# Kernel tuning notes

Hardware: AMD Instinct MI355X
Metric: run time of the kernel (lower is better)

## Reference

```python
import jax, jax.numpy as jnp
import numpy as np

HIDDEN = 128
HEADS = 8
HEAD_DIM = HIDDEN // HEADS
N_NODES = 100000
N_EDGES = 1600000


def setup_inputs() -> dict:
    key = jax.random.key(0)
    ks = jax.random.split(key, 12)
    s = 1.0 / np.sqrt(HIDDEN)
    inp = {
        "x": jax.random.normal(ks[0], (N_NODES, HIDDEN), dtype=jnp.float32),
        "edge_index": jax.random.randint(ks[1], (2, N_EDGES), 0, N_NODES, dtype=jnp.int32),
        "edge_emb": jax.random.normal(ks[2], (N_EDGES, HIDDEN), dtype=jnp.float32),
        "q_w": jax.random.uniform(ks[3], (HIDDEN, HIDDEN), jnp.float32, -s, s),
        "q_b": jax.random.uniform(ks[4], (HIDDEN,), jnp.float32, -s, s),
        "k_w": jax.random.uniform(ks[5], (HIDDEN, HIDDEN), jnp.float32, -s, s),
        "k_b": jax.random.uniform(ks[6], (HIDDEN,), jnp.float32, -s, s),
        "v_w": jax.random.uniform(ks[7], (HIDDEN, HIDDEN), jnp.float32, -s, s),
        "v_b": jax.random.uniform(ks[8], (HIDDEN,), jnp.float32, -s, s),
        "out_w": jax.random.uniform(ks[9], (HIDDEN, HIDDEN), jnp.float32, -s, s),
        "out_b": jax.random.uniform(ks[10], (HIDDEN,), jnp.float32, -s, s),
        "eb_w": jax.random.uniform(ks[11], (HEADS, HIDDEN), jnp.float32, -s, s),
        "eb_b": jnp.zeros((HEADS,), dtype=jnp.float32),
    }
    return inp


def reference(x, edge_index, edge_emb, q_w, q_b, k_w, k_b, v_w, v_b, out_w, out_b, eb_w, eb_b):
    n = x.shape[0]
    # node projections -> [N, H, D]
    q = (x @ q_w.T + q_b).reshape(n, HEADS, HEAD_DIM)
    k = (x @ k_w.T + k_b).reshape(n, HEADS, HEAD_DIM)
    v = (x @ v_w.T + v_b).reshape(n, HEADS, HEAD_DIM)

    row, col = edge_index[0], edge_index[1]
    # per-edge scores: [E, H]
    scores = jnp.einsum('ehd,ehd->eh', q[row], k[col]) / jnp.sqrt(jnp.float32(HEAD_DIM))
    scores = scores + edge_emb @ eb_w.T + eb_b

    # segmented softmax over incoming edges of each destination node `row`
    seg_max = jax.ops.segment_max(scores, row, num_segments=n)  # [N, H]
    exp_scores = jnp.exp(scores - seg_max[row])
    seg_sum = jax.ops.segment_sum(exp_scores, row, num_segments=n)  # [N, H]
    attn = exp_scores / (seg_sum[row] + 1e-10)  # [E, H]

    # weighted scatter-aggregation of values
    weighted_v = attn[..., None] * v[col]  # [E, H, D]
    out = jax.ops.segment_sum(weighted_v, row, num_segments=n)  # [N, H, D]
    out = out.reshape(n, HIDDEN)
    return out @ out_w.T + out_b
```

## Files before the change

### kernel.cpp

```cpp
#include <hip/hip_runtime.h>

#define HID 128
#define NH 8

typedef __attribute__((ext_vector_type(8))) short short8;
typedef __attribute__((ext_vector_type(4))) float f32x4;

__device__ __forceinline__ unsigned short f2bf(float f) {
    unsigned int u = __float_as_uint(f);
    u = (u + 0x7FFF + ((u >> 16) & 1)) >> 16;
    return (unsigned short)u;
}
__device__ __forceinline__ float bf2f(unsigned short s) {
    return __uint_as_float((unsigned int)s << 16);
}

__global__ void k_hist(const int* __restrict__ row, int E, int* __restrict__ count) {
    int i = blockIdx.x * blockDim.x + threadIdx.x;
    int stride = gridDim.x * blockDim.x;
    for (; i < E; i += stride) atomicAdd(&count[row[i]], 1);
}

__global__ void k_scan1(const int* __restrict__ in, int total,
                        int* __restrict__ out, int* __restrict__ bsums) {
    __shared__ int sd[256];
    int t = threadIdx.x;
    int base = blockIdx.x * 1024 + t * 4;
    int v0 = (base + 0 < total) ? in[base + 0] : 0;
    int v1 = (base + 1 < total) ? in[base + 1] : 0;
    int v2 = (base + 2 < total) ? in[base + 2] : 0;
    int v3 = (base + 3 < total) ? in[base + 3] : 0;
    int s = v0 + v1 + v2 + v3;
    sd[t] = s; __syncthreads();
    for (int off = 1; off < 256; off <<= 1) {
        int xx = (t >= off) ? sd[t - off] : 0;
        __syncthreads();
        sd[t] += xx;
        __syncthreads();
    }
    int excl = sd[t] - s;
    if (t == 255) bsums[blockIdx.x] = sd[255];
    int run = excl;
    if (base + 0 < total) out[base + 0] = run; run += v0;
    if (base + 1 < total) out[base + 1] = run; run += v1;
    if (base + 2 < total) out[base + 2] = run; run += v2;
    if (base + 3 < total) out[base + 3] = run;
}

__global__ void k_scan2(int* __restrict__ bs, int nb) {
    __shared__ int sd[128];
    int t = threadIdx.x;
    int vv = (t < nb) ? bs[t] : 0;
    sd[t] = vv; __syncthreads();
    for (int off = 1; off < 128; off <<= 1) {
        int xx = (t >= off) ? sd[t - off] : 0;
        __syncthreads();
        sd[t] += xx;
        __syncthreads();
    }
    if (t < nb) bs[t] = sd[t] - vv;
}

__global__ void k_scan3(int* __restrict__ out, int total, const int* __restrict__ bs) {
    int add = bs[blockIdx.x];
    int base = blockIdx.x * 1024 + threadIdx.x * 4;
    #pragma unroll
    for (int i = 0; i < 4; ++i)
        if (base + i < total) out[base + i] += add;
}

__global__ __launch_bounds__(256) void k_edge_fused(
    const int* __restrict__ row, const int* __restrict__ col,
    const float* __restrict__ emb, const float* __restrict__ ebw,
    const float* __restrict__ ebb, const int* __restrict__ start,
    int* __restrict__ cursor, int* __restrict__ col_sorted,
    float* __restrict__ ebias_s, int E)
{
    __shared__ float Wx[8][4][8][4];
    __shared__ float bb[8];
    int t = threadIdx.x;
    for (int i = t; i < 1024; i += 256) {
        int j = i & 3, g = (i >> 2) & 7, c = (i >> 5) & 3, h = i >> 7;
        Wx[h][c][g][j] = ebw[h * 128 + g * 16 + c * 4 + j];
    }
    if (t < 8) bb[t] = ebb[t];
    __syncthreads();

    int l = t & 63;
    int g = l & 7;
    int sub = l >> 3;
    int wid = blockIdx.x * 4 + (t >> 6);
    int nwaves = gridDim.x * 4;

    for (int base = wid * 8; base < E; base += nwaves * 8) {
        int e = base + sub;
        bool act = e < E;
        float p[8] = {0.f,0.f,0.f,0.f,0.f,0.f,0.f,0.f};
        if (act) {
            const float4* pe = (const float4*)(emb + (size_t)e * HID + g * 16);
            #pragma unroll
            for (int c = 0; c < 4; ++c) {
                float4 ev = pe[c];
                #pragma unroll
                for (int h = 0; h < 8; ++h) {
                    float4 wv = *(const float4*)&Wx[h][c][g][0];
                    p[h] += ev.x*wv.x + ev.y*wv.y + ev.z*wv.z + ev.w*wv.w;
                }
            }
        }
        #pragma unroll
        for (int off = 1; off < 8; off <<= 1) {
            #pragma unroll
            for (int h = 0; h < 8; ++h) p[h] += __shfl_xor(p[h], off);
        }
        int pslot = 0;
        if (act && g == 0) {
            int r = row[e];
            pslot = start[r] + atomicAdd(&cursor[r], 1);
            col_sorted[pslot] = col[e];
        }
        pslot = __shfl(pslot, l & 56);
        if (act) ebias_s[(size_t)pslot * NH + g] = p[g] + bb[g];
    }
}

__global__ void k_cvtw(const float* __restrict__ qw, const float* __restrict__ kw,
                       const float* __restrict__ vw, const float* __restrict__ ow,
                       unsigned short* __restrict__ wbf) {
    int i = blockIdx.x * 256 + threadIdx.x;
    int idx = i * 4;
    int m = idx >> 14;
    int off = idx & 16383;
    const float* src = (m == 0) ? qw : (m == 1) ? kw : (m == 2) ? vw : ow;
    float4 v = *(const float4*)(src + off);
    ushort4 o;
    o.x = f2bf(v.x); o.y = f2bf(v.y); o.z = f2bf(v.z); o.w = f2bf(v.w);
    *(ushort4*)(wbf + idx) = o;
}

__global__ __launch_bounds__(256) void k_qkv_mfma(
    const float* __restrict__ x, const unsigned short* __restrict__ wbf,
    const float* __restrict__ qb, const float* __restrict__ kb, const float* __restrict__ vb,
    unsigned short* __restrict__ qkvbf, int n)
{
    __shared__ unsigned short xs[64][136];
    int t = threadIdx.x;
    int m0 = blockIdx.x * 64;
    #pragma unroll
    for (int p = 0; p < 2; ++p) {
        int f = p * 256 + t;
        int r = f >> 3;
        int c16 = (f & 7) * 16;
        int node = m0 + r;
        float4 u0 = {0,0,0,0}, u1 = {0,0,0,0}, u2 = {0,0,0,0}, u3 = {0,0,0,0};
        if (node < n) {
            const float4* px = (const float4*)(x + (size_t)node * HID + c16);
            u0 = px[0]; u1 = px[1]; u2 = px[2]; u3 = px[3];
        }
        union { unsigned short u[8]; short8 v; } a, b;
        a.u[0]=f2bf(u0.x); a.u[1]=f2bf(u0.y); a.u[2]=f2bf(u0.z); a.u[3]=f2bf(u0.w);
        a.u[4]=f2bf(u1.x); a.u[5]=f2bf(u1.y); a.u[6]=f2bf(u1.z); a.u[7]=f2bf(u1.w);
        b.u[0]=f2bf(u2.x); b.u[1]=f2bf(u2.y); b.u[2]=f2bf(u2.z); b.u[3]=f2bf(u2.w);
        b.u[4]=f2bf(u3.x); b.u[5]=f2bf(u3.y); b.u[6]=f2bf(u3.z); b.u[7]=f2bf(u3.w);
        *(short8*)&xs[r][c16]     = a.v;
        *(short8*)&xs[r][c16 + 8] = b.v;
    }
    __syncthreads();

    int w = t >> 6, l = t & 63;
    int lr = l & 15, lc = l >> 4;
    short8 afr[4];
    #pragma unroll
    for (int c = 0; c < 4; ++c)
        afr[c] = *(const short8*)&xs[w * 16 + lr][c * 32 + lc * 8];

    #pragma unroll
    for (int m = 0; m < 3; ++m) {
        const float* bias = (m == 0) ? qb : (m == 1) ? kb : vb;
        #pragma unroll
        for (int ct = 0; ct < 8; ++ct) {
            int colg = ct * 16 + lr;
            f32x4 acc = {0.f, 0.f, 0.f, 0.f};
            const unsigned short* wrow = wbf + (size_t)m * 16384 + (size_t)colg * 128 + lc * 8;
            #pragma unroll
            for (int c = 0; c < 4; ++c) {
                short8 bfr = *(const short8*)(wrow + c * 32);
                acc = __builtin_amdgcn_mfma_f32_16x16x32_bf16(afr[c], bfr, acc, 0, 0, 0);
            }
            float bv = bias[colg];
            #pragma unroll
            for (int r = 0; r < 4; ++r) {
                int node = m0 + w * 16 + lc * 4 + r;
                if (node < n)
                    qkvbf[(size_t)node * 384 + m * 128 + colg] = f2bf(acc[r] + bv);
            }
        }
    }
}

__global__ __launch_bounds__(256) void k_attn(
    const unsigned short* __restrict__ qkvbf, const float* __restrict__ ebs,
    const int* __restrict__ cols, const int* __restrict__ start,
    float* __restrict__ out, int n)
{
    int node = blockIdx.x * 4 + (threadIdx.x >> 6);
    if (node >= n) return;
    int l = threadIdx.x & 63;
    int slot = l >> 3;
    int h = l & 7;
    int s0 = start[node];
    int deg = start[node + 1] - s0;

    float qf[16];
    {
        const unsigned short* qp = qkvbf + (size_t)node * 384 + h * 16;
        short8 q0 = *(const short8*)qp;
        short8 q1 = *(const short8*)(qp + 8);
        #pragma unroll
        for (int i = 0; i < 8; ++i) {
            qf[i] = bf2f((unsigned short)q0[i]);
            qf[8 + i] = bf2f((unsigned short)q1[i]);
        }
    }

    float acc[16];
    #pragma unroll
    for (int i = 0; i < 16; ++i) acc[i] = 0.f;
    float denom = 0.f;

    for (int base = 0; base < deg; base += 8) {
        int idx = base + slot;
        bool act = idx < deg;
        int c = act ? cols[s0 + idx] : 0;
        const unsigned short* kv = qkvbf + (size_t)c * 384 + 128 + h * 16;
        short8 ka  = *(const short8*)kv;
        short8 kbv = *(const short8*)(kv + 8);
        short8 va  = *(const short8*)(kv + 128);
        short8 vb  = *(const short8*)(kv + 136);
        float eb = act ? ebs[(size_t)(s0 + idx) * NH + h] : 0.f;
        float part = 0.f;
        #pragma unroll
        for (int i = 0; i < 8; ++i) part += qf[i] * bf2f((unsigned short)ka[i]);
        #pragma unroll
        for (int i = 0; i < 8; ++i) part += qf[8 + i] * bf2f((unsigned short)kbv[i]);
        float es = act ? __expf(part * 0.25f + eb) : 0.f;
        denom += es;
        #pragma unroll
        for (int i = 0; i < 8; ++i) acc[i]     += es * bf2f((unsigned short)va[i]);
        #pragma unroll
        for (int i = 0; i < 8; ++i) acc[8 + i] += es * bf2f((unsigned short)vb[i]);
    }

    #pragma unroll
    for (int off = 8; off < 64; off <<= 1) {
        denom += __shfl_xor(denom, off);
        #pragma unroll
        for (int i = 0; i < 16; ++i) acc[i] += __shfl_xor(acc[i], off);
    }
    if (slot == 0) {
        float inv = 1.f / (denom + 1e-10f);
        float* op = out + (size_t)node * HID + h * 16;
        #pragma unroll
        for (int c = 0; c < 4; ++c) {
            float4 o = make_float4(acc[c*4]*inv, acc[c*4+1]*inv, acc[c*4+2]*inv, acc[c*4+3]*inv);
            *(float4*)(op + c * 4) = o;
        }
    }
}

__global__ __launch_bounds__(256) void k_outproj_mfma(
    float* __restrict__ io, const unsigned short* __restrict__ wbf,
    const float* __restrict__ ob, int n)
{
    __shared__ unsigned short hs[64][136];
    int t = threadIdx.x;
    int m0 = blockIdx.x * 64;
    #pragma unroll
    for (int p = 0; p < 2; ++p) {
        int f = p * 256 + t;
        int r = f >> 3;
        int c16 = (f & 7) * 16;
        int node = m0 + r;
        float4 u0 = {0,0,0,0}, u1 = {0,0,0,0}, u2 = {0,0,0,0}, u3 = {0,0,0,0};
        if (node < n) {
            const float4* px = (const float4*)(io + (size_t)node * HID + c16);
            u0 = px[0]; u1 = px[1]; u2 = px[2]; u3 = px[3];
        }
        union { unsigned short u[8]; short8 v; } a, b;
        a.u[0]=f2bf(u0.x); a.u[1]=f2bf(u0.y); a.u[2]=f2bf(u0.z); a.u[3]=f2bf(u0.w);
        a.u[4]=f2bf(u1.x); a.u[5]=f2bf(u1.y); a.u[6]=f2bf(u1.z); a.u[7]=f2bf(u1.w);
        b.u[0]=f2bf(u2.x); b.u[1]=f2bf(u2.y); b.u[2]=f2bf(u2.z); b.u[3]=f2bf(u2.w);
        b.u[4]=f2bf(u3.x); b.u[5]=f2bf(u3.y); b.u[6]=f2bf(u3.z); b.u[7]=f2bf(u3.w);
        *(short8*)&hs[r][c16]     = a.v;
        *(short8*)&hs[r][c16 + 8] = b.v;
    }
    __syncthreads();

    int w = t >> 6, l = t & 63;
    int lr = l & 15, lc = l >> 4;
    short8 afr[4];
    #pragma unroll
    for (int c = 0; c < 4; ++c)
        afr[c] = *(const short8*)&hs[w * 16 + lr][c * 32 + lc * 8];

    #pragma unroll
    for (int ct = 0; ct < 8; ++ct) {
        int colg = ct * 16 + lr;
        f32x4 acc = {0.f, 0.f, 0.f, 0.f};
        const unsigned short* wrow = wbf + (size_t)3 * 16384 + (size_t)colg * 128 + lc * 8;
        #pragma unroll
        for (int c = 0; c < 4; ++c) {
            short8 bfr = *(const short8*)(wrow + c * 32);
            acc = __builtin_amdgcn_mfma_f32_16x16x32_bf16(afr[c], bfr, acc, 0, 0, 0);
        }
        float bv = ob[colg];
        #pragma unroll
        for (int r = 0; r < 4; ++r) {
            int node = m0 + w * 16 + lc * 4 + r;
            if (node < n)
                io[(size_t)node * HID + colg] = acc[r] + bv;
        }
    }
}

extern "C" void kernel_launch(void* const* d_in, const int* in_sizes, int n_in,
                              void* d_out, int out_size, void* d_ws, size_t ws_size,
                              hipStream_t stream) {
    const float* x   = (const float*)d_in[0];
    const int*   eix = (const int*)  d_in[1];
    const float* emb = (const float*)d_in[2];
    const float* qw  = (const float*)d_in[3];
    const float* qb  = (const float*)d_in[4];
    const float* kw  = (const float*)d_in[5];
    const float* kb  = (const float*)d_in[6];
    const float* vw  = (const float*)d_in[7];
    const float* vb  = (const float*)d_in[8];
    const float* ow  = (const float*)d_in[9];
    const float* ob  = (const float*)d_in[10];
    const float* ebw = (const float*)d_in[11];
    const float* ebb = (const float*)d_in[12];

    int n = in_sizes[0] / HID;
    int E = in_sizes[2] / HID;
    const int* row = eix;
    const int* col = eix + E;

    char* wsp = (char*)d_ws;
    auto alloc = [&](size_t bytes) -> void* {
        void* p = (void*)wsp;
        wsp += (bytes + 255) & ~(size_t)255;
        return p;
    };
    unsigned short* qkvbf = (unsigned short*)alloc((size_t)n * 384 * 2);
    unsigned short* wbf   = (unsigned short*)alloc((size_t)4 * 16384 * 2);
    float* ebias_s        = (float*)alloc((size_t)E * NH * 4);
    int* count            = (int*)alloc((size_t)(n + 2) * 4);
    int* startp           = (int*)alloc((size_t)(n + 2) * 4);
    int* bsums            = (int*)alloc(256 * 4);
    int* cursor           = (int*)alloc((size_t)n * 4);
    int* col_sorted       = (int*)alloc((size_t)E * 4);

    hipMemsetAsync(count, 0, (size_t)(n + 1) * sizeof(int), stream);
    hipMemsetAsync(cursor, 0, (size_t)n * sizeof(int), stream);

    k_cvtw<<<64, 256, 0, stream>>>(qw, kw, vw, ow, wbf);
    k_hist<<<2048, 256, 0, stream>>>(row, E, count);

    int total = n + 1;
    int nb = (total + 1023) / 1024;
    k_scan1<<<nb, 256, 0, stream>>>(count, total, startp, bsums);
    k_scan2<<<1, 128, 0, stream>>>(bsums, nb);
    k_scan3<<<nb, 256, 0, stream>>>(startp, total, bsums);

    k_edge_fused<<<2048, 256, 0, stream>>>(row, col, emb, ebw, ebb, startp,
                                           cursor, col_sorted, ebias_s, E);

    k_qkv_mfma<<<(n + 63) / 64, 256, 0, stream>>>(x, wbf, qb, kb, vb, qkvbf, n);
    k_attn<<<(n + 3) / 4, 256, 0, stream>>>(qkvbf, ebias_s, col_sorted, startp,
                                            (float*)d_out, n);
    k_outproj_mfma<<<(n + 63) / 64, 256, 0, stream>>>((float*)d_out, wbf, ob, n);
}
```

Baseline: 570.4 us.

## Fuse QKV projection and edge-bias pass; pack edge records, bf16 attention output

Merges the QKV projection and the edge-bias/scatter kernel into one launch with block-range dispatch, so the two independent stages run concurrently. The edge scatter now writes a 32-byte record per edge holding the column index and the eight biases as bf16, replacing the separate col_sorted and fp32 ebias arrays, so attention reads one record instead of two scattered values. Attention writes its output as bf16 into a scratch buffer that the output projection reads directly, removing an fp32 round trip and a conversion. Storing the edge bias and aggregated output in bf16 costs some precision, and the edge pass now uses one 32-edge block per launch slot instead of a grid-stride loop.

```diff
diff --git a/kernel.cpp b/kernel.cpp
--- a/kernel.cpp
+++ b/kernel.cpp
@@ -13,6 +13,9 @@
 }
 __device__ __forceinline__ float bf2f(unsigned short s) {
     return __uint_as_float((unsigned int)s << 16);
+}
+__device__ __forceinline__ unsigned int pack2bf(float lo, float hi) {
+    return (unsigned int)f2bf(lo) | ((unsigned int)f2bf(hi) << 16);
 }
 
 __global__ void k_hist(const int* __restrict__ row, int E, int* __restrict__ count) {
@@ -69,32 +72,103 @@
         if (base + i < total) out[base + i] += add;
 }
 
-__global__ __launch_bounds__(256) void k_edge_fused(
+__global__ void k_cvtw(const float* __restrict__ qw, const float* __restrict__ kw,
+                       const float* __restrict__ vw, const float* __restrict__ ow,
+                       unsigned short* __restrict__ wbf) {
+    int i = blockIdx.x * 256 + threadIdx.x;
+    int idx = i * 4;
+    int m = idx >> 14;
+    int off = idx & 16383;
+    const float* src = (m == 0) ? qw : (m == 1) ? kw : (m == 2) ? vw : ow;
+    float4 v = *(const float4*)(src + off);
+    ushort4 o;
+    o.x = f2bf(v.x); o.y = f2bf(v.y); o.z = f2bf(v.z); o.w = f2bf(v.w);
+    *(ushort4*)(wbf + idx) = o;
+}
+
+__global__ __launch_bounds__(256) void k_fat(
+    const float* __restrict__ x, const unsigned short* __restrict__ wbf,
+    const float* __restrict__ qb_, const float* __restrict__ kb_, const float* __restrict__ vb_,
+    unsigned short* __restrict__ qkvbf, int n, int qblocks,
     const int* __restrict__ row, const int* __restrict__ col,
     const float* __restrict__ emb, const float* __restrict__ ebw,
     const float* __restrict__ ebb, const int* __restrict__ start,
-    int* __restrict__ cursor, int* __restrict__ col_sorted,
-    float* __restrict__ ebias_s, int E)
+    int* __restrict__ cursor, char* __restrict__ recs, int E)
 {
-    __shared__ float Wx[8][4][8][4];
-    __shared__ float bb[8];
+    __shared__ __align__(16) char sm[17408];
+    int bid = blockIdx.x;
     int t = threadIdx.x;
-    for (int i = t; i < 1024; i += 256) {
-        int j = i & 3, g = (i >> 2) & 7, c = (i >> 5) & 3, h = i >> 7;
-        Wx[h][c][g][j] = ebw[h * 128 + g * 16 + c * 4 + j];
-    }
-    if (t < 8) bb[t] = ebb[t];
-    __syncthreads();
-
-    int l = t & 63;
-    int g = l & 7;
-    int sub = l >> 3;
-    int wid = blockIdx.x * 4 + (t >> 6);
-    int nwaves = gridDim.x * 4;
-
-    for (int base = wid * 8; base < E; base += nwaves * 8) {
-        int e = base + sub;
+
+    if (bid < qblocks) {
+        unsigned short (*xs)[136] = (unsigned short (*)[136])sm;
+        int m0 = bid * 64;
+        #pragma unroll
+        for (int p = 0; p < 2; ++p) {
+            int f = p * 256 + t;
+            int r = f >> 3;
+            int c16 = (f & 7) * 16;
+            int node = m0 + r;
+            float4 u0 = {0,0,0,0}, u1 = {0,0,0,0}, u2 = {0,0,0,0}, u3 = {0,0,0,0};
+            if (node < n) {
+                const float4* px = (const float4*)(x + (size_t)node * HID + c16);
+                u0 = px[0]; u1 = px[1]; u2 = px[2]; u3 = px[3];
+            }
+            union { unsigned short u[8]; short8 v; } a, b;
+            a.u[0]=f2bf(u0.x); a.u[1]=f2bf(u0.y); a.u[2]=f2bf(u0.z); a.u[3]=f2bf(u0.w);
+            a.u[4]=f2bf(u1.x); a.u[5]=f2bf(u1.y); a.u[6]=f2bf(u1.z); a.u[7]=f2bf(u1.w);
+            b.u[0]=f2bf(u2.x); b.u[1]=f2bf(u2.y); b.u[2]=f2bf(u2.z); b.u[3]=f2bf(u2.w);
+            b.u[4]=f2bf(u3.x); b.u[5]=f2bf(u3.y); b.u[6]=f2bf(u3.z); b.u[7]=f2bf(u3.w);
+            *(short8*)&xs[r][c16]     = a.v;
+            *(short8*)&xs[r][c16 + 8] = b.v;
+        }
+        __syncthreads();
+
+        int w = t >> 6, l = t & 63;
+        int lr = l & 15, lc = l >> 4;
+        short8 afr[4];
+        #pragma unroll
+        for (int c = 0; c < 4; ++c)
+            afr[c] = *(const short8*)&xs[w * 16 + lr][c * 32 + lc * 8];
+
+        #pragma unroll
+        for (int m = 0; m < 3; ++m) {
+            const float* bias = (m == 0) ? qb_ : (m == 1) ? kb_ : vb_;
+            #pragma unroll
+            for (int ct = 0; ct < 8; ++ct) {
+                int colg = ct * 16 + lr;
+                f32x4 acc = {0.f, 0.f, 0.f, 0.f};
+                const unsigned short* wrow = wbf + (size_t)m * 16384 + (size_t)colg * 128 + lc * 8;
+                #pragma unroll
+                for (int c = 0; c < 4; ++c) {
+                    short8 bfr = *(const short8*)(wrow + c * 32);
+                    acc = __builtin_amdgcn_mfma_f32_16x16x32_bf16(afr[c], bfr, acc, 0, 0, 0);
+                }
+                float bv = bias[colg];
+                #pragma unroll
+                for (int r = 0; r < 4; ++r) {
+                    int node = m0 + w * 16 + lc * 4 + r;
+                    if (node < n)
+                        qkvbf[(size_t)node * 384 + m * 128 + colg] = f2bf(acc[r] + bv);
+                }
+            }
+        }
+    } else {
+        float (*Wx)[4][8][4] = (float (*)[4][8][4])sm;
+        for (int i = t; i < 1024; i += 256) {
+            int j = i & 3, g = (i >> 2) & 7, c = (i >> 5) & 3, h = i >> 7;
+            Wx[h][c][g][j] = ebw[h * 128 + g * 16 + c * 4 + j];
+        }
+        float bbr[8];
+        #pragma unroll
+        for (int i = 0; i < 8; ++i) bbr[i] = ebb[i];
+        __syncthreads();
+
+        int l = t & 63;
+        int g = l & 7;
+        int sub = l >> 3;
+        int e = (bid - qblocks) * 32 + (t >> 6) * 8 + sub;
         bool act = e < E;
+
         float p[8] = {0.f,0.f,0.f,0.f,0.f,0.f,0.f,0.f};
         if (act) {
             const float4* pe = (const float4*)(emb + (size_t)e * HID + g * 16);
@@ -113,95 +187,27 @@
             #pragma unroll
             for (int h = 0; h < 8; ++h) p[h] += __shfl_xor(p[h], off);
         }
-        int pslot = 0;
         if (act && g == 0) {
             int r = row[e];
-            pslot = start[r] + atomicAdd(&cursor[r], 1);
-            col_sorted[pslot] = col[e];
-        }
-        pslot = __shfl(pslot, l & 56);
-        if (act) ebias_s[(size_t)pslot * NH + g] = p[g] + bb[g];
-    }
-}
-
-__global__ void k_cvtw(const float* __restrict__ qw, const float* __restrict__ kw,
-                       const float* __restrict__ vw, const float* __restrict__ ow,
-                       unsigned short* __restrict__ wbf) {
-    int i = blockIdx.x * 256 + threadIdx.x;
-    int idx = i * 4;
-    int m = idx >> 14;
-    int off = idx & 16383;
-    const float* src = (m == 0) ? qw : (m == 1) ? kw : (m == 2) ? vw : ow;
-    float4 v = *(const float4*)(src + off);
-    ushort4 o;
-    o.x = f2bf(v.x); o.y = f2bf(v.y); o.z = f2bf(v.z); o.w = f2bf(v.w);
-    *(ushort4*)(wbf + idx) = o;
-}
-
-__global__ __launch_bounds__(256) void k_qkv_mfma(
-    const float* __restrict__ x, const unsigned short* __restrict__ wbf,
-    const float* __restrict__ qb, const float* __restrict__ kb, const float* __restrict__ vb,
-    unsigned short* __restrict__ qkvbf, int n)
-{
-    __shared__ unsigned short xs[64][136];
-    int t = threadIdx.x;
-    int m0 = blockIdx.x * 64;
-    #pragma unroll
-    for (int p = 0; p < 2; ++p) {
-        int f = p * 256 + t;
-        int r = f >> 3;
-        int c16 = (f & 7) * 16;
-        int node = m0 + r;
-        float4 u0 = {0,0,0,0}, u1 = {0,0,0,0}, u2 = {0,0,0,0}, u3 = {0,0,0,0};
-        if (node < n) {
-            const float4* px = (const float4*)(x + (size_t)node * HID + c16);
-            u0 = px[0]; u1 = px[1]; u2 = px[2]; u3 = px[3];
-        }
-        union { unsigned short u[8]; short8 v; } a, b;
-        a.u[0]=f2bf(u0.x); a.u[1]=f2bf(u0.y); a.u[2]=f2bf(u0.z); a.u[3]=f2bf(u0.w);
-        a.u[4]=f2bf(u1.x); a.u[5]=f2bf(u1.y); a.u[6]=f2bf(u1.z); a.u[7]=f2bf(u1.w);
-        b.u[0]=f2bf(u2.x); b.u[1]=f2bf(u2.y); b.u[2]=f2bf(u2.z); b.u[3]=f2bf(u2.w);
-        b.u[4]=f2bf(u3.x); b.u[5]=f2bf(u3.y); b.u[6]=f2bf(u3.z); b.u[7]=f2bf(u3.w);
-        *(short8*)&xs[r][c16]     = a.v;
-        *(short8*)&xs[r][c16 + 8] = b.v;
-    }
-    __syncthreads();
-
-    int w = t >> 6, l = t & 63;
-    int lr = l & 15, lc = l >> 4;
-    short8 afr[4];
-    #pragma unroll
-    for (int c = 0; c < 4; ++c)
-        afr[c] = *(const short8*)&xs[w * 16 + lr][c * 32 + lc * 8];
-
-    #pragma unroll
-    for (int m = 0; m < 3; ++m) {
-        const float* bias = (m == 0) ? qb : (m == 1) ? kb : vb;
-        #pragma unroll
-        for (int ct = 0; ct < 8; ++ct) {
-            int colg = ct * 16 + lr;
-            f32x4 acc = {0.f, 0.f, 0.f, 0.f};
-            const unsigned short* wrow = wbf + (size_t)m * 16384 + (size_t)colg * 128 + lc * 8;
-            #pragma unroll
-            for (int c = 0; c < 4; ++c) {
-                short8 bfr = *(const short8*)(wrow + c * 32);
-                acc = __builtin_amdgcn_mfma_f32_16x16x32_bf16(afr[c], bfr, acc, 0, 0, 0);
-            }
-            float bv = bias[colg];
-            #pragma unroll
-            for (int r = 0; r < 4; ++r) {
-                int node = m0 + w * 16 + lc * 4 + r;
-                if (node < n)
-                    qkvbf[(size_t)node * 384 + m * 128 + colg] = f2bf(acc[r] + bv);
-            }
+            int ps = start[r] + atomicAdd(&cursor[r], 1);
+            char* rp = recs + (size_t)ps * 32;
+            uint4 r0;
+            r0.x = (unsigned int)col[e];
+            r0.y = pack2bf(p[0] + bbr[0], p[1] + bbr[1]);
+            r0.z = pack2bf(p[2] + bbr[2], p[3] + bbr[3]);
+            r0.w = pack2bf(p[4] + bbr[4], p[5] + bbr[5]);
+            uint2 r1;
+            r1.x = pack2bf(p[6] + bbr[6], p[7] + bbr[7]);
+            r1.y = 0;
+            *(uint4*)rp = r0;
+            *(uint2*)(rp + 16) = r1;
         }
     }
 }
 
 __global__ __launch_bounds__(256) void k_attn(
-    const unsigned short* __restrict__ qkvbf, const float* __restrict__ ebs,
-    const int* __restrict__ cols, const int* __restrict__ start,
-    float* __restrict__ out, int n)
+    const unsigned short* __restrict__ qkvbf, const char* __restrict__ recs,
+    const int* __restrict__ start, unsigned short* __restrict__ aout, int n)
 {
     int node = blockIdx.x * 4 + (threadIdx.x >> 6);
     if (node >= n) return;
@@ -231,13 +237,14 @@
     for (int base = 0; base < deg; base += 8) {
         int idx = base + slot;
         bool act = idx < deg;
-        int c = act ? cols[s0 + idx] : 0;
+        const char* rp = recs + (size_t)(s0 + (act ? idx : 0)) * 32;
+        int c = act ? *(const int*)rp : 0;
+        float eb = act ? bf2f(*(const unsigned short*)(rp + 4 + 2 * h)) : 0.f;
         const unsigned short* kv = qkvbf + (size_t)c * 384 + 128 + h * 16;
         short8 ka  = *(const short8*)kv;
         short8 kbv = *(const short8*)(kv + 8);
         short8 va  = *(const short8*)(kv + 128);
         short8 vb  = *(const short8*)(kv + 136);
-        float eb = act ? ebs[(size_t)(s0 + idx) * NH + h] : 0.f;
         float part = 0.f;
         #pragma unroll
         for (int i = 0; i < 8; ++i) part += qf[i] * bf2f((unsigned short)ka[i]);
@@ -259,40 +266,37 @@
     }
     if (slot == 0) {
         float inv = 1.f / (denom + 1e-10f);
-        float* op = out + (size_t)node * HID + h * 16;
-        #pragma unroll
-        for (int c = 0; c < 4; ++c) {
-            float4 o = make_float4(acc[c*4]*inv, acc[c*4+1]*inv, acc[c*4+2]*inv, acc[c*4+3]*inv);
-            *(float4*)(op + c * 4) = o;
-        }
+        uint4 o0, o1;
+        o0.x = pack2bf(acc[0]*inv,  acc[1]*inv);
+        o0.y = pack2bf(acc[2]*inv,  acc[3]*inv);
+        o0.z = pack2bf(acc[4]*inv,  acc[5]*inv);
+        o0.w = pack2bf(acc[6]*inv,  acc[7]*inv);
+        o1.x = pack2bf(acc[8]*inv,  acc[9]*inv);
+        o1.y = pack2bf(acc[10]*inv, acc[11]*inv);
+        o1.z = pack2bf(acc[12]*inv, acc[13]*inv);
+        o1.w = pack2bf(acc[14]*inv, acc[15]*inv);
+        unsigned short* op = aout + (size_t)node * HID + h * 16;
+        *(uint4*)op       = o0;
+        *(uint4*)(op + 8) = o1;
     }
 }
 
 __global__ __launch_bounds__(256) void k_outproj_mfma(
-    float* __restrict__ io, const unsigned short* __restrict__ wbf,
-    const float* __restrict__ ob, int n)
+    const unsigned short* __restrict__ aout, const unsigned short* __restrict__ wbf,
+    const float* __restrict__ ob, float* __restrict__ out, int n)
 {
     __shared__ unsigned short hs[64][136];
     int t = threadIdx.x;
     int m0 = blockIdx.x * 64;
     #pragma unroll
-    for (int p = 0; p < 2; ++p) {
+    for (int p = 0; p < 4; ++p) {
         int f = p * 256 + t;
-        int r = f >> 3;
-        int c16 = (f & 7) * 16;
+        int r = f >> 4;
+        int c8 = (f & 15) * 8;
         int node = m0 + r;
-        float4 u0 = {0,0,0,0}, u1 = {0,0,0,0}, u2 = {0,0,0,0}, u3 = {0,0,0,0};
-        if (node < n) {
-            const float4* px = (const float4*)(io + (size_t)node * HID + c16);
-            u0 = px[0]; u1 = px[1]; u2 = px[2]; u3 = px[3];
-        }
-        union { unsigned short u[8]; short8 v; } a, b;
-        a.u[0]=f2bf(u0.x); a.u[1]=f2bf(u0.y); a.u[2]=f2bf(u0.z); a.u[3]=f2bf(u0.w);
-        a.u[4]=f2bf(u1.x); a.u[5]=f2bf(u1.y); a.u[6]=f2bf(u1.z); a.u[7]=f2bf(u1.w);
-        b.u[0]=f2bf(u2.x); b.u[1]=f2bf(u2.y); b.u[2]=f2bf(u2.z); b.u[3]=f2bf(u2.w);
-        b.u[4]=f2bf(u3.x); b.u[5]=f2bf(u3.y); b.u[6]=f2bf(u3.z); b.u[7]=f2bf(u3.w);
-        *(short8*)&hs[r][c16]     = a.v;
-        *(short8*)&hs[r][c16 + 8] = b.v;
+        short8 val = {0,0,0,0,0,0,0,0};
+        if (node < n) val = *(const short8*)(aout + (size_t)node * HID + c8);
+        *(short8*)&hs[r][c8] = val;
     }
     __syncthreads();
 
@@ -318,7 +322,7 @@
         for (int r = 0; r < 4; ++r) {
             int node = m0 + w * 16 + lc * 4 + r;
             if (node < n)
-                io[(size_t)node * HID + colg] = acc[r] + bv;
+                out[(size_t)node * HID + colg] = acc[r] + bv;
         }
     }
 }
@@ -353,12 +357,12 @@
     };
     unsigned short* qkvbf = (unsigned short*)alloc((size_t)n * 384 * 2);
     unsigned short* wbf   = (unsigned short*)alloc((size_t)4 * 16384 * 2);
-    float* ebias_s        = (float*)alloc((size_t)E * NH * 4);
+    char* recs            = (char*)alloc((size_t)E * 32);
+    unsigned short* aout  = (unsigned short*)alloc((size_t)n * HID * 2);
     int* count            = (int*)alloc((size_t)(n + 2) * 4);
     int* startp           = (int*)alloc((size_t)(n + 2) * 4);
     int* bsums            = (int*)alloc(256 * 4);
     int* cursor           = (int*)alloc((size_t)n * 4);
-    int* col_sorted       = (int*)alloc((size_t)E * 4);
 
     hipMemsetAsync(count, 0, (size_t)(n + 1) * sizeof(int), stream);
     hipMemsetAsync(cursor, 0, (size_t)n * sizeof(int), stream);
@@ -372,11 +376,12 @@
     k_scan2<<<1, 128, 0, stream>>>(bsums, nb);
     k_scan3<<<nb, 256, 0, stream>>>(startp, total, bsums);
 
-    k_edge_fused<<<2048, 256, 0, stream>>>(row, col, emb, ebw, ebb, startp,
-                                           cursor, col_sorted, ebias_s, E);
-
-    k_qkv_mfma<<<(n + 63) / 64, 256, 0, stream>>>(x, wbf, qb, kb, vb, qkvbf, n);
-    k_attn<<<(n + 3) / 4, 256, 0, stream>>>(qkvbf, ebias_s, col_sorted, startp,
-                                            (float*)d_out, n);
-    k_outproj_mfma<<<(n + 63) / 64, 256, 0, stream>>>((float*)d_out, wbf, ob, n);
-}
+    int qblocks = (n + 63) / 64;
+    int eblocks = (E + 31) / 32;
+    k_fat<<<qblocks + eblocks, 256, 0, stream>>>(
+        x, wbf, qb, kb, vb, qkvbf, n, qblocks,
+        row, col, emb, ebw, ebb, startp, cursor, recs, E);
+
+    k_attn<<<(n + 3) / 4, 256, 0, stream>>>(qkvbf, recs, startp, aout, n);
+    k_outproj_mfma<<<(n + 63) / 64, 256, 0, stream>>>(aout, wbf, ob, (float*)d_out, n);
+}
```

Result: no change. 564.3 us (-1.1%).
